# Kernel tuning notes

Hardware: AMD Instinct MI355X
Metric: run time of the kernel (lower is better)

## Reference

```python
import jax, jax.numpy as jnp
import numpy as np

D_MODEL = 1024
N_HEADS = 16
HEAD_DIM = D_MODEL // N_HEADS
NEG_INF = -1e30


def _rotary(v):
    # v: [B, H, T, hd]. Original module rotates each (even, odd) pair by 90 deg:
    # out[..., 2i] = -v[..., 2i+1]; out[..., 2i+1] = v[..., 2i]
    v2 = v.reshape(*v.shape[:-1], HEAD_DIM // 2, 2)
    return jnp.stack([-v2[..., 1], v2[..., 0]], axis=-1).reshape(v.shape)


def setup_inputs() -> dict:
    key = jax.random.key(0)
    ks = jax.random.split(key, 9)
    B, T, D = 2, 2048, D_MODEL
    s = 1.0 / np.sqrt(D)
    inp = {
        "x": jax.random.normal(ks[0], (B, T, D), dtype=jnp.float32),
        "Wq_w": jax.random.normal(ks[1], (D, D), dtype=jnp.float32) * s,
        "Wq_b": jnp.zeros((D,), dtype=jnp.float32),
        "Wk_w": jax.random.normal(ks[2], (D, D), dtype=jnp.float32) * s,
        "Wk_b": jnp.zeros((D,), dtype=jnp.float32),
        "Wv_w": jax.random.normal(ks[3], (D, D), dtype=jnp.float32) * s,
        "Wv_b": jnp.zeros((D,), dtype=jnp.float32),
        "Wo_w": jax.random.normal(ks[4], (D, D), dtype=jnp.float32) * s,
        "Wo_b": jnp.zeros((D,), dtype=jnp.float32),
    }
    # create_sparse_mask: block-diagonal True windows of size T//4
    window = T // 4
    blk = jnp.arange(T) // window
    inp["sparse_mask"] = blk[:, None] == blk[None, :]
    return inp


def reference(x, Wq_w, Wq_b, Wk_w, Wk_b, Wv_w, Wv_b, Wo_w, Wo_b, sparse_mask):
    B, T, D = x.shape
    H, hd = N_HEADS, HEAD_DIM

    def proj(w, b):  # [B,T,D] -> [B,H,T,hd]
        return (x @ w.T + b).reshape(B, T, H, hd).transpose(0, 2, 1, 3)

    q = _rotary(proj(Wq_w, Wq_b))
    k = _rotary(proj(Wk_w, Wk_b))
    v = proj(Wv_w, Wv_b)

    scores = jnp.einsum("bhqd,bhkd->bhqk", q, k) / jnp.sqrt(jnp.asarray(hd, x.dtype))
    causal = jnp.tril(jnp.ones((T, T), dtype=bool))
    allowed = sparse_mask & causal  # block-diagonal AND causal
    scores = jnp.where(allowed, scores, NEG_INF)
    attn = jax.nn.softmax(scores, axis=-1)  # dropout_p=0.1 omitted (eval mode)
    out = jnp.einsum("bhqk,bhkd->bhqd", attn, v)
    out = out.transpose(0, 2, 1, 3).reshape(B, T, D)
    return out @ Wo_w.T + Wo_b
```

## Files before the change

### kernel.cpp

```cpp
#include <hip/hip_runtime.h>
#include <hip/hip_bf16.h>
#include <stdint.h>

typedef __attribute__((ext_vector_type(4))) float f32x4;
typedef __attribute__((ext_vector_type(8))) __bf16 bf16x8;
typedef __attribute__((ext_vector_type(4))) unsigned short u16x4;
typedef __attribute__((ext_vector_type(8))) unsigned short u16x8;
typedef __attribute__((ext_vector_type(2))) unsigned int u32x2;
typedef const __attribute__((address_space(1))) void* as1_cvp;
typedef __attribute__((address_space(3))) void* as3_vp;

#define LOG2E 1.44269504088896340736f

#define VMW0() asm volatile("s_waitcnt vmcnt(0)" ::: "memory")
#define BAR()  do { __builtin_amdgcn_sched_barrier(0); __builtin_amdgcn_s_barrier(); \
                    __builtin_amdgcn_sched_barrier(0); } while (0)

static __device__ __forceinline__ unsigned short f2bf(float f) {
  union { float f; unsigned int u; } c; c.f = f;
  unsigned int r = c.u + 0x7FFFu + ((c.u >> 16) & 1u);
  return (unsigned short)(r >> 16);
}

static __device__ __forceinline__ void gl_lds16(const void* g, void* l) {
  __builtin_amdgcn_global_load_lds((as1_cvp)(uintptr_t)g, (as3_vp)(uintptr_t)l, 16, 0, 0);
}

__global__ __launch_bounds__(256) void cvt_kernel(
    const float* __restrict__ x, const float* __restrict__ wq, const float* __restrict__ wk,
    const float* __restrict__ wv, const float* __restrict__ wo,
    unsigned short* __restrict__ xb, unsigned short* __restrict__ wqb,
    unsigned short* __restrict__ wkb, unsigned short* __restrict__ wvb,
    unsigned short* __restrict__ wob) {
  long e = ((long)blockIdx.x * 256 + threadIdx.x) * 8;
  const float* s; unsigned short* d; long o;
  if (e < 4194304)      { s = x;  d = xb;  o = e; }
  else if (e < 5242880) { s = wq; d = wqb; o = e - 4194304; }
  else if (e < 6291456) { s = wk; d = wkb; o = e - 5242880; }
  else if (e < 7340032) { s = wv; d = wvb; o = e - 6291456; }
  else                  { s = wo; d = wob; o = e - 7340032; }
  float4 a = *(const float4*)(s + o);
  float4 b = *(const float4*)(s + o + 4);
  u16x8 v;
  v[0] = f2bf(a.x); v[1] = f2bf(a.y); v[2] = f2bf(a.z); v[3] = f2bf(a.w);
  v[4] = f2bf(b.x); v[5] = f2bf(b.y); v[6] = f2bf(b.z); v[7] = f2bf(b.w);
  *(u16x8*)(d + o) = v;
}

__global__ __launch_bounds__(512, 6) void gemm_qkv8(
    const unsigned short* __restrict__ xb, const unsigned short* __restrict__ wcat,
    const float* __restrict__ bq, const float* __restrict__ bk, const float* __restrict__ bv,
    unsigned short* __restrict__ qo, unsigned short* __restrict__ ko,
    unsigned short* __restrict__ vto) {
  __shared__ __align__(16) char lds[32768];
  const int tid = threadIdx.x;
  const int lane = tid & 63, wid = tid >> 6;
  const int wm = wid >> 2, wn = wid & 3;
  const int c = lane & 15, g = lane >> 4;

  const int bid = blockIdx.x;
  const int xcd = bid & 7, idx = bid >> 3;
  const int m0 = (((xcd & 1) << 4) + idx / 6) << 7;
  const int n0 = (((xcd >> 1) * 6) + idx % 6) << 7;

  const int sj = tid >> 3;
  const int sg = (tid & 7) ^ (sj & 7);
  const long soff = (((long)(sj + ((sg >> 2) << 6))) << 11) + ((sg & 3) << 4);
  const char* Ab = (const char*)xb;
  const char* Bb = (const char*)wcat;

  const int sA = ((((wm << 2) | g) ^ (c & 7)) << 4);
  const int sB = (((((wn >> 1) << 2) | g) ^ (c & 7)) << 4);
  const char* pAr = lds + (c << 7) + sA;
  const char* pBr = lds + 8192 + ((((wn & 1) << 5) + c) << 7) + sB;

  f32x4 acc[4][2] = {};

  auto STAGE = [&](int t, int slot) {
    char* db = lds + slot * 16384;
    const long ko = (long)t << 6;
    gl_lds16(Ab + ((long)m0 << 11) + soff + ko, db + tid * 16);
    gl_lds16(Bb + ((long)n0 << 11) + soff + ko, db + 8192 + tid * 16);
  };

  STAGE(0, 0);

#pragma unroll 1
  for (int t = 0; t < 32; ++t) {
    VMW0();
    BAR();
    if (t + 1 < 32) STAGE(t + 1, (t + 1) & 1);

    const int sb = (t & 1) * 16384;
    bf16x8 aa[4];
#pragma unroll
    for (int f = 0; f < 4; ++f) aa[f] = *(const bf16x8*)(pAr + sb + (f << 11));
    bf16x8 bb0 = *(const bf16x8*)(pBr + sb);
    bf16x8 bb1 = *(const bf16x8*)(pBr + sb + 2048);
    __builtin_amdgcn_s_setprio(1);
#pragma unroll
    for (int f = 0; f < 4; ++f)
      acc[f][0] = __builtin_amdgcn_mfma_f32_16x16x32_bf16(aa[f], bb0, acc[f][0], 0, 0, 0);
#pragma unroll
    for (int f = 0; f < 4; ++f)
      acc[f][1] = __builtin_amdgcn_mfma_f32_16x16x32_bf16(aa[f], bb1, acc[f][1], 0, 0, 0);
    __builtin_amdgcn_s_setprio(0);
  }

#pragma unroll
  for (int nf = 0; nf < 2; ++nf) {
    const int n = n0 + (wn << 5) + (nf << 4) + c;
    const int z = n >> 10, nn = n & 1023;
    const float bb_ = (z == 0 ? bq : z == 1 ? bk : bv)[nn];
    const float sc = (z == 0) ? 0.125f : 1.0f;
    const int h = nn >> 6, dd = nn & 63;
#pragma unroll
    for (int f = 0; f < 4; ++f) {
      const int mb = m0 + (wm << 6) + (f << 4) + (g << 2);
      const int b = mb >> 11, tt = mb & 2047;
      if (z < 2) {
        unsigned short* dst = (z == 0 ? qo : ko) +
            ((((long)(b << 4) + h) << 11) + tt) * 64 + dd;
#pragma unroll
        for (int j = 0; j < 4; ++j) dst[(long)j * 64] = f2bf((acc[f][nf][j] + bb_) * sc);
      } else {
        u16x4 pk;
#pragma unroll
        for (int j = 0; j < 4; ++j) pk[j] = f2bf(acc[f][nf][j] + bb_);
        *(u16x4*)(vto + ((((long)((b << 4) + h) << 6) + dd) << 11) + tt) = pk;
      }
    }
  }
}

__global__ __launch_bounds__(512, 4) void gemm_oproj8(
    const unsigned short* __restrict__ ab, const unsigned short* __restrict__ wob,
    const float* __restrict__ bo, float* __restrict__ out) {
  __shared__ __align__(16) char lds[49152];
  const int tid = threadIdx.x;
  const int lane = tid & 63, wid = tid >> 6;
  const int wm = wid >> 2, wn = wid & 3;
  const int c = lane & 15, g = lane >> 4;

  const int bid = blockIdx.x;
  const int xcd = bid & 7, idx = bid >> 3;
  const int m0 = ((xcd << 3) + (idx >> 3)) << 6;
  const int n0 = (idx & 7) << 7;

  const int srow = tid >> 3;
  const int coff = (((tid & 7) ^ (srow & 7)) << 4);
  const char* Ab = (const char*)ab;
  const char* Bb = (const char*)wob;

  const int swzr0 = ((g ^ (c & 7)) << 4);
  const int swzr1 = (((4 | g) ^ (c & 7)) << 4);

  f32x4 acc[2][2] = {};

  auto STAGE = [&](int kt, int unit) {
    char* db = lds + (kt & 1) * 24576;
    const char* gp; char* dst;
    if (unit == 0) {
      gp = Ab + ((long)(m0 + srow) << 11) + (kt << 7) + coff;
      dst = db + tid * 16;
    } else {
      gp = Bb + ((long)(n0 + (unit - 1) * 64 + srow) << 11) + (kt << 7) + coff;
      dst = db + unit * 8192 + tid * 16;
    }
    gl_lds16(gp, dst);
  };

  STAGE(0, 0); STAGE(0, 1); STAGE(0, 2);
  VMW0();
  BAR();

#pragma unroll 1
  for (int kt = 0; kt < 16; ++kt) {
    const int bufb = (kt & 1) * 24576;
    if (kt < 15) { STAGE(kt + 1, 0); STAGE(kt + 1, 1); STAGE(kt + 1, 2); }
    bf16x8 aa[2][2];
    const char* pA = lds + bufb + (wm << 12) + (c << 7);
#pragma unroll
    for (int f = 0; f < 2; ++f) {
      aa[f][0] = *(const bf16x8*)(pA + (f << 11) + swzr0);
      aa[f][1] = *(const bf16x8*)(pA + (f << 11) + swzr1);
    }
#pragma unroll
    for (int nf = 0; nf < 2; ++nf) {
      const int rB = (wn << 5) + (nf << 4) + c;
      const char* pB = lds + bufb + 8192 + ((rB >> 6) << 13) + ((rB & 63) << 7);
      bf16x8 b0 = *(const bf16x8*)(pB + swzr0);
      bf16x8 b1 = *(const bf16x8*)(pB + swzr1);
      __builtin_amdgcn_s_setprio(1);
#pragma unroll
      for (int f = 0; f < 2; ++f)
        acc[f][nf] = __builtin_amdgcn_mfma_f32_16x16x32_bf16(aa[f][0], b0, acc[f][nf], 0, 0, 0);
#pragma unroll
      for (int f = 0; f < 2; ++f)
        acc[f][nf] = __builtin_amdgcn_mfma_f32_16x16x32_bf16(aa[f][1], b1, acc[f][nf], 0, 0, 0);
      __builtin_amdgcn_s_setprio(0);
    }
    if (kt < 15) VMW0();
    BAR();
  }

#pragma unroll
  for (int nf = 0; nf < 2; ++nf) {
    const int n = n0 + (wn << 5) + (nf << 4) + c;
    const float bb = bo[n];
#pragma unroll
    for (int f = 0; f < 2; ++f) {
      const int mb = m0 + (wm << 5) + (f << 4) + (g << 2);
#pragma unroll
      for (int j = 0; j < 4; ++j)
        out[((long)(mb + j) << 10) + n] = acc[f][nf][j] + bb;
    }
  }
}

__global__ __launch_bounds__(512, 6) void attn_kernel(
    const unsigned short* __restrict__ qg, const unsigned short* __restrict__ kg,
    const unsigned short* __restrict__ vtg, unsigned short* __restrict__ og) {
  __shared__ __align__(16) char kv_s[2][16384];
  __shared__ __align__(16) char p_s[8][2304];

  const int bx = blockIdx.x, bh = blockIdx.y;
  const int map1[16] = {3,7,11,15, 2,6,10,14, 0,4,8,12, 1,5,9,13};
  const int map2[16] = {0,4,8,12, 1,5,9,13, 3,7,11,15, 2,6,10,14};
  const int qt = (bh < 16) ? map1[bx] : map2[bx];
  const int tid = threadIdx.x;
  const int lane = tid & 63, w = tid >> 6;
  const int c = lane & 15, g = lane >> 4;
  const int q0 = qt << 7;
  const int wstart = q0 & ~511;
  const int nt = ((q0 - wstart) >> 6) + 2;

  const unsigned short* qrow = qg + (((long)bh << 11) + q0 + (w << 4) + c) * 64;
  bf16x8 qa0 = *(const bf16x8*)(qrow + (g << 3));
  bf16x8 qa1 = *(const bf16x8*)(qrow + (g << 3) + 32);

  float m_run = -3.0e38f, l_run = 0.0f;
  f32x4 oacc[4] = {};

  const int sr = tid >> 3;
  const int jx16 = (((tid & 7) ^ (sr & 7)) << 4);
  const char* kbase = (const char*)kg + ((((long)bh << 11) + sr) << 7) + jx16;
  const char* vbase = (const char*)vtg + ((((long)bh << 6) + sr) << 12) + jx16;
  const int t16 = tid << 4;

  auto STAGEKV = [&](int kv0, int bsel) {
    char* dst = kv_s[bsel];
    gl_lds16(kbase + ((long)kv0 << 7), dst + t16);
    gl_lds16(vbase + ((long)kv0 << 1), dst + 8192 + t16);
  };

  STAGEKV(wstart, 0);

  for (int t = 0; t < nt; ++t) {
    VMW0();
    BAR();
    if (t + 1 < nt) STAGEKV(wstart + ((t + 1) << 6), (t + 1) & 1);

    const char* kb_ = kv_s[t & 1];
    const char* vb_ = kv_s[t & 1] + 8192;
    const int kv0 = wstart + (t << 6);

    f32x4 sacc[4] = {};
    __builtin_amdgcn_s_setprio(1);
#pragma unroll
    for (int mf = 0; mf < 4; ++mf) {
      const int kr = (mf << 4) + c;
      const char* kp = kb_ + (kr << 7);
      bf16x8 k0 = *(const bf16x8*)(kp + ((g ^ (kr & 7)) << 4));
      bf16x8 k1 = *(const bf16x8*)(kp + (((4 | g) ^ (kr & 7)) << 4));
      sacc[mf] = __builtin_amdgcn_mfma_f32_16x16x32_bf16(k0, qa0, sacc[mf], 0, 0, 0);
      sacc[mf] = __builtin_amdgcn_mfma_f32_16x16x32_bf16(k1, qa1, sacc[mf], 0, 0, 0);
    }
    __builtin_amdgcn_s_setprio(0);

    const int dkv = kv0 - q0;
    if (dkv > (w << 4) - 64) {
      const int qrel = (w << 4) + c;
#pragma unroll
      for (int mf = 0; mf < 4; ++mf)
#pragma unroll
        for (int j = 0; j < 4; ++j)
          if (dkv + (mf << 4) + (g << 2) + j > qrel) sacc[mf][j] = -3.0e38f;
    }

    float pm[4];
#pragma unroll
    for (int mf = 0; mf < 4; ++mf)
      pm[mf] = fmaxf(fmaxf(sacc[mf][0], sacc[mf][1]), fmaxf(sacc[mf][2], sacc[mf][3]));
    float pmax = fmaxf(fmaxf(pm[0], pm[1]), fmaxf(pm[2], pm[3]));
    pmax = fmaxf(pmax, __shfl_xor(pmax, 16));
    pmax = fmaxf(pmax, __shfl_xor(pmax, 32));

    const bool resc = !__all(pmax <= m_run + 8.0f);
    const float m_new = resc ? fmaxf(m_run, pmax) : m_run;

    const float mL = m_new * LOG2E;
    float ls[4];
#pragma unroll
    for (int mf = 0; mf < 4; ++mf) {
      float p0 = __builtin_amdgcn_exp2f(__builtin_fmaf(sacc[mf][0], LOG2E, -mL));
      float p1 = __builtin_amdgcn_exp2f(__builtin_fmaf(sacc[mf][1], LOG2E, -mL));
      float p2 = __builtin_amdgcn_exp2f(__builtin_fmaf(sacc[mf][2], LOG2E, -mL));
      float p3 = __builtin_amdgcn_exp2f(__builtin_fmaf(sacc[mf][3], LOG2E, -mL));
      sacc[mf][0] = p0; sacc[mf][1] = p1; sacc[mf][2] = p2; sacc[mf][3] = p3;
      ls[mf] = (p0 + p1) + (p2 + p3);
    }
    float lsum = (ls[0] + ls[1]) + (ls[2] + ls[3]);
    lsum += __shfl_xor(lsum, 16);
    lsum += __shfl_xor(lsum, 32);

    if (resc) {
      const float alpha = __builtin_amdgcn_exp2f((m_run - m_new) * LOG2E);
      l_run *= alpha;
#pragma unroll
      for (int j = 0; j < 4; ++j) {
        const float aj = __shfl(alpha, (g << 2) + j);
#pragma unroll
        for (int nf = 0; nf < 4; ++nf) oacc[nf][j] *= aj;
      }
      m_run = m_new;
    }
    l_run += lsum;

    {
      char* pw = p_s[w] + c * 144;
#pragma unroll
      for (int mf = 0; mf < 4; ++mf) {
        unsigned int p01, p23;
        asm("v_cvt_pk_bf16_f32 %0, %1, %2" : "=v"(p01) : "v"(sacc[mf][0]), "v"(sacc[mf][1]));
        asm("v_cvt_pk_bf16_f32 %0, %1, %2" : "=v"(p23) : "v"(sacc[mf][2]), "v"(sacc[mf][3]));
        u32x2 pk; pk[0] = p01; pk[1] = p23;
        *(u32x2*)(pw + (mf << 5) + (g << 3)) = pk;
      }
    }

    const char* pr = p_s[w] + c * 144;
    __builtin_amdgcn_s_setprio(1);
#pragma unroll
    for (int kk = 0; kk < 2; ++kk) {
      bf16x8 pa = *(const bf16x8*)(pr + (kk << 6) + (g << 4));
#pragma unroll
      for (int nf = 0; nf < 4; ++nf) {
        const int vr = (nf << 4) + c;
        bf16x8 vb = *(const bf16x8*)(vb_ + (vr << 7) +
                                     ((((kk << 2) | g) ^ (vr & 7)) << 4));
        oacc[nf] = __builtin_amdgcn_mfma_f32_16x16x32_bf16(pa, vb, oacc[nf], 0, 0, 0);
      }
    }
    __builtin_amdgcn_s_setprio(0);
  }

  const int b = bh >> 4, h = bh & 15;
#pragma unroll
  for (int j = 0; j < 4; ++j) {
    const float linv = 1.0f / __shfl(l_run, (g << 2) + j);
    const int trow = q0 + (w << 4) + (g << 2) + j;
    unsigned short* dst = og + ((((long)(b << 11)) + trow) << 10) + (h << 6);
#pragma unroll
    for (int nf = 0; nf < 4; ++nf)
      dst[(nf << 4) + c] = f2bf(oacc[nf][j] * linv);
  }
}

extern "C" void kernel_launch(void* const* d_in, const int* in_sizes, int n_in,
                              void* d_out, int out_size, void* d_ws, size_t ws_size,
                              hipStream_t stream) {
  const float* x  = (const float*)d_in[0];
  const float* wq = (const float*)d_in[1];
  const float* bq = (const float*)d_in[2];
  const float* wk = (const float*)d_in[3];
  const float* bk = (const float*)d_in[4];
  const float* wv = (const float*)d_in[5];
  const float* bv = (const float*)d_in[6];
  const float* wo = (const float*)d_in[7];
  const float* bo = (const float*)d_in[8];

  char* ws = (char*)d_ws;
  unsigned short* xb    = (unsigned short*)(ws);
  unsigned short* wqb   = (unsigned short*)(ws + 8388608);
  unsigned short* wkb   = (unsigned short*)(ws + 10485760);
  unsigned short* wvb   = (unsigned short*)(ws + 12582912);
  unsigned short* wob   = (unsigned short*)(ws + 14680064);
  unsigned short* qb    = (unsigned short*)(ws + 16777216);
  unsigned short* kb    = (unsigned short*)(ws + 25165824);
  unsigned short* vtb   = (unsigned short*)(ws + 33554432);
  unsigned short* attnb = xb;

  cvt_kernel<<<4096, 256, 0, stream>>>(x, wq, wk, wv, wo, xb, wqb, wkb, wvb, wob);
  gemm_qkv8<<<768, 512, 0, stream>>>(xb, wqb, bq, bk, bv, qb, kb, vtb);
  attn_kernel<<<dim3(16, 32), 512, 0, stream>>>(qb, kb, vtb, attnb);
  gemm_oproj8<<<512, 512, 0, stream>>>(attnb, wob, bo, (float*)d_out);
}
```

Baseline: 79.59 us.

## Enlarge QKV GEMM tiles to 256x256 with deeper quarter-staged LDS pipeline

Measured after the change: 78.63 us. Within noise of the previous version (-1.2%).

```diff
diff --git a/kernel.cpp b/kernel.cpp
--- a/kernel.cpp
+++ b/kernel.cpp
@@ -13,8 +13,12 @@
 #define LOG2E 1.44269504088896340736f
 
 #define VMW0() asm volatile("s_waitcnt vmcnt(0)" ::: "memory")
+#define VMW6() asm volatile("s_waitcnt vmcnt(6)" ::: "memory")
 #define BAR()  do { __builtin_amdgcn_sched_barrier(0); __builtin_amdgcn_s_barrier(); \
                     __builtin_amdgcn_sched_barrier(0); } while (0)
+#define SB()   __builtin_amdgcn_s_barrier()
+#define LGKM0() do { asm volatile("s_waitcnt lgkmcnt(0)" ::: "memory"); \
+                     __builtin_amdgcn_sched_barrier(0); } while (0)
 
 static __device__ __forceinline__ unsigned short f2bf(float f) {
   union { float f; unsigned int u; } c; c.f = f;
@@ -47,86 +51,129 @@
   *(u16x8*)(d + o) = v;
 }
 
-__global__ __launch_bounds__(512, 6) void gemm_qkv8(
+__global__ __launch_bounds__(512, 2) void gemm_qkv8(
     const unsigned short* __restrict__ xb, const unsigned short* __restrict__ wcat,
     const float* __restrict__ bq, const float* __restrict__ bk, const float* __restrict__ bv,
     unsigned short* __restrict__ qo, unsigned short* __restrict__ ko,
     unsigned short* __restrict__ vto) {
-  __shared__ __align__(16) char lds[32768];
+  __shared__ __align__(16) char lds[131072];
   const int tid = threadIdx.x;
   const int lane = tid & 63, wid = tid >> 6;
   const int wm = wid >> 2, wn = wid & 3;
   const int c = lane & 15, g = lane >> 4;
 
   const int bid = blockIdx.x;
-  const int xcd = bid & 7, idx = bid >> 3;
-  const int m0 = (((xcd & 1) << 4) + idx / 6) << 7;
-  const int n0 = (((xcd >> 1) * 6) + idx % 6) << 7;
-
-  const int sj = tid >> 3;
-  const int sg = (tid & 7) ^ (sj & 7);
-  const long soff = (((long)(sj + ((sg >> 2) << 6))) << 11) + ((sg & 3) << 4);
+  const int swz = (bid & 7) * 24 + (bid >> 3);
+  const int n0 = (swz % 12) << 8;
+  const int m0 = (swz / 12) << 8;
+
+  const int srow = tid >> 3;
+  const int coff = (((tid & 7) ^ (srow & 7)) << 4);
   const char* Ab = (const char*)xb;
   const char* Bb = (const char*)wcat;
 
-  const int sA = ((((wm << 2) | g) ^ (c & 7)) << 4);
-  const int sB = (((((wn >> 1) << 2) | g) ^ (c & 7)) << 4);
-  const char* pAr = lds + (c << 7) + sA;
-  const char* pBr = lds + 8192 + ((((wn & 1) << 5) + c) << 7) + sB;
-
-  f32x4 acc[4][2] = {};
-
-  auto STAGE = [&](int t, int slot) {
-    char* db = lds + slot * 16384;
-    const long ko = (long)t << 6;
-    gl_lds16(Ab + ((long)m0 << 11) + soff + ko, db + tid * 16);
-    gl_lds16(Bb + ((long)n0 << 11) + soff + ko, db + 8192 + tid * 16);
-  };
-
-  STAGE(0, 0);
+  const int swzr0 = ((g ^ (c & 7)) << 4);
+  const int swzr1 = (((4 | g) ^ (c & 7)) << 4);
+  const int aRow = ((wm << 6) + c) << 7;
+  const int bRow = 32768 + (((wn << 5) + c) << 7);
+
+  f32x4 acc[8][4] = {};
+  bf16x8 aa[4][2], bb[2][2][2];
+
+  auto STAGE = [&](int H) {
+    const int part = H & 3, kt = H >> 2;
+    char* db = lds + ((kt & 1) << 16);
+    const char* mat; int rb, reg;
+    if (part == 0)      { mat = Ab; rb = m0;       reg = 0; }
+    else if (part == 1) { mat = Bb; rb = n0;       reg = 32768; }
+    else if (part == 2) { mat = Bb; rb = n0 + 128; reg = 49152; }
+    else                { mat = Ab; rb = m0 + 128; reg = 16384; }
+    const char* gp = mat + ((long)(rb + srow) << 11) + (kt << 7) + coff;
+    gl_lds16(gp,               db + reg + tid * 16);
+    gl_lds16(gp + (64l << 11), db + reg + 8192 + tid * 16);
+  };
+  auto RDA = [&](int bufb, int half) {
+    const char* p = lds + bufb + (half << 14) + aRow;
+#pragma unroll
+    for (int m4 = 0; m4 < 4; ++m4) {
+      aa[m4][0] = *(const bf16x8*)(p + (m4 << 11) + swzr0);
+      aa[m4][1] = *(const bf16x8*)(p + (m4 << 11) + swzr1);
+    }
+  };
+  auto RDB = [&](int bufb, int half) {
+    const char* p = lds + bufb + (half << 14) + bRow;
+#pragma unroll
+    for (int n2 = 0; n2 < 2; ++n2) {
+      bb[half][n2][0] = *(const bf16x8*)(p + (n2 << 11) + swzr0);
+      bb[half][n2][1] = *(const bf16x8*)(p + (n2 << 11) + swzr1);
+    }
+  };
+  auto MM = [&](int mh, int nh) {
+    __builtin_amdgcn_s_setprio(1);
+#pragma unroll
+    for (int m4 = 0; m4 < 4; ++m4)
+#pragma unroll
+      for (int n2 = 0; n2 < 2; ++n2)
+#pragma unroll
+        for (int kf = 0; kf < 2; ++kf)
+          acc[mh * 4 + m4][nh * 2 + n2] = __builtin_amdgcn_mfma_f32_16x16x32_bf16(
+              aa[m4][kf], bb[nh][n2][kf], acc[mh * 4 + m4][nh * 2 + n2], 0, 0, 0);
+    __builtin_amdgcn_s_setprio(0);
+  };
+
+  STAGE(0); STAGE(1); STAGE(2); STAGE(3); STAGE(4);
+  VMW6();
+  SB();
 
 #pragma unroll 1
-  for (int t = 0; t < 32; ++t) {
-    VMW0();
-    BAR();
-    if (t + 1 < 32) STAGE(t + 1, (t + 1) & 1);
-
-    const int sb = (t & 1) * 16384;
-    bf16x8 aa[4];
-#pragma unroll
-    for (int f = 0; f < 4; ++f) aa[f] = *(const bf16x8*)(pAr + sb + (f << 11));
-    bf16x8 bb0 = *(const bf16x8*)(pBr + sb);
-    bf16x8 bb1 = *(const bf16x8*)(pBr + sb + 2048);
-    __builtin_amdgcn_s_setprio(1);
-#pragma unroll
-    for (int f = 0; f < 4; ++f)
-      acc[f][0] = __builtin_amdgcn_mfma_f32_16x16x32_bf16(aa[f], bb0, acc[f][0], 0, 0, 0);
-#pragma unroll
-    for (int f = 0; f < 4; ++f)
-      acc[f][1] = __builtin_amdgcn_mfma_f32_16x16x32_bf16(aa[f], bb1, acc[f][1], 0, 0, 0);
-    __builtin_amdgcn_s_setprio(0);
-  }
-
-#pragma unroll
-  for (int nf = 0; nf < 2; ++nf) {
-    const int n = n0 + (wn << 5) + (nf << 4) + c;
+  for (int kt = 0; kt < 16; ++kt) {
+    const int bufb = (kt & 1) << 16;
+    const int GP = kt << 2;
+    RDA(bufb, 0); RDB(bufb, 0);
+    STAGE(GP + 5);
+    VMW6();
+    SB(); LGKM0();
+    MM(0, 0);
+    SB();
+    RDB(bufb, 1);
+    STAGE(GP + 6);
+    VMW6();
+    SB(); LGKM0();
+    MM(0, 1);
+    SB();
+    RDA(bufb, 1);
+    STAGE(GP + 7);
+    SB(); LGKM0();
+    MM(1, 1);
+    SB();
+    STAGE(GP + 8);
+    VMW6();
+    SB(); LGKM0();
+    MM(1, 0);
+    SB();
+  }
+  VMW0();
+
+#pragma unroll
+  for (int nf = 0; nf < 4; ++nf) {
+    const int n = n0 + ((nf >> 1) << 7) + (wn << 5) + ((nf & 1) << 4) + c;
     const int z = n >> 10, nn = n & 1023;
     const float bb_ = (z == 0 ? bq : z == 1 ? bk : bv)[nn];
     const float sc = (z == 0) ? 0.125f : 1.0f;
     const int h = nn >> 6, dd = nn & 63;
 #pragma unroll
-    for (int f = 0; f < 4; ++f) {
-      const int mb = m0 + (wm << 6) + (f << 4) + (g << 2);
+    for (int mf = 0; mf < 8; ++mf) {
+      const int mb = m0 + ((mf >> 2) << 7) + (wm << 6) + ((mf & 3) << 4) + (g << 2);
       const int b = mb >> 11, tt = mb & 2047;
       if (z < 2) {
         unsigned short* dst = (z == 0 ? qo : ko) +
             ((((long)(b << 4) + h) << 11) + tt) * 64 + dd;
 #pragma unroll
-        for (int j = 0; j < 4; ++j) dst[(long)j * 64] = f2bf((acc[f][nf][j] + bb_) * sc);
+        for (int j = 0; j < 4; ++j) dst[(long)j * 64] = f2bf((acc[mf][nf][j] + bb_) * sc);
       } else {
         u16x4 pk;
 #pragma unroll
-        for (int j = 0; j < 4; ++j) pk[j] = f2bf(acc[f][nf][j] + bb_);
+        for (int j = 0; j < 4; ++j) pk[j] = f2bf(acc[mf][nf][j] + bb_);
         *(u16x4*)(vto + ((((long)((b << 4) + h) << 6) + dd) << 11) + tt) = pk;
       }
     }
@@ -392,7 +439,7 @@
   unsigned short* attnb = xb;
 
   cvt_kernel<<<4096, 256, 0, stream>>>(x, wq, wk, wv, wo, xb, wqb, wkb, wvb, wob);
-  gemm_qkv8<<<768, 512, 0, stream>>>(xb, wqb, bq, bk, bv, qb, kb, vtb);
+  gemm_qkv8<<<192, 512, 0, stream>>>(xb, wqb, bq, bk, bv, qb, kb, vtb);
   attn_kernel<<<dim3(16, 32), 512, 0, stream>>>(qb, kb, vtb, attnb);
   gemm_oproj8<<<512, 512, 0, stream>>>(attnb, wob, bo, (float*)d_out);
 }
```

## Rework QKV GEMM to 256-thread blocks with 64x64 warp tiles, single-buffered

Applied to the files above, without the earlier changes.

New measurement: 80.29 us. Within noise of the previous version (+0.9%).

```diff
diff --git a/kernel.cpp b/kernel.cpp
--- a/kernel.cpp
+++ b/kernel.cpp
@@ -47,86 +47,80 @@
   *(u16x8*)(d + o) = v;
 }
 
-__global__ __launch_bounds__(512, 6) void gemm_qkv8(
+__global__ __launch_bounds__(256, 3) void gemm_qkv97(
     const unsigned short* __restrict__ xb, const unsigned short* __restrict__ wcat,
     const float* __restrict__ bq, const float* __restrict__ bk, const float* __restrict__ bv,
     unsigned short* __restrict__ qo, unsigned short* __restrict__ ko,
     unsigned short* __restrict__ vto) {
-  __shared__ __align__(16) char lds[32768];
+  __shared__ __align__(16) char lds[16384];
   const int tid = threadIdx.x;
   const int lane = tid & 63, wid = tid >> 6;
-  const int wm = wid >> 2, wn = wid & 3;
+  const int wm = wid >> 1, wn = wid & 1;
   const int c = lane & 15, g = lane >> 4;
 
   const int bid = blockIdx.x;
   const int xcd = bid & 7, idx = bid >> 3;
-  const int m0 = (((xcd & 1) << 4) + idx / 6) << 7;
-  const int n0 = (((xcd >> 1) * 6) + idx % 6) << 7;
+  const int m0 = (((xcd >> 1) << 3) + idx / 12) << 7;
+  const int n0 = (((xcd & 1) * 12) + idx % 12) << 7;
 
   const int sj = tid >> 3;
   const int sg = (tid & 7) ^ (sj & 7);
-  const long soff = (((long)(sj + ((sg >> 2) << 6))) << 11) + ((sg & 3) << 4);
-  const char* Ab = (const char*)xb;
-  const char* Bb = (const char*)wcat;
+  const long rowoff = ((long)(sj + ((sg >> 2) << 6)) << 11) + ((sg & 3) << 4);
+  const char* Ag = (const char*)xb   + ((long)m0 << 11) + rowoff;
+  const char* Bg = (const char*)wcat + ((long)n0 << 11) + rowoff;
 
   const int sA = ((((wm << 2) | g) ^ (c & 7)) << 4);
-  const int sB = (((((wn >> 1) << 2) | g) ^ (c & 7)) << 4);
+  const int sB = ((((wn << 2) | g) ^ (c & 7)) << 4);
   const char* pAr = lds + (c << 7) + sA;
-  const char* pBr = lds + 8192 + ((((wn & 1) << 5) + c) << 7) + sB;
-
-  f32x4 acc[4][2] = {};
-
-  auto STAGE = [&](int t, int slot) {
-    char* db = lds + slot * 16384;
-    const long ko = (long)t << 6;
-    gl_lds16(Ab + ((long)m0 << 11) + soff + ko, db + tid * 16);
-    gl_lds16(Bb + ((long)n0 << 11) + soff + ko, db + 8192 + tid * 16);
-  };
-
-  STAGE(0, 0);
+  const char* pBr = lds + 8192 + (c << 7) + sB;
+
+  f32x4 acc[4][4] = {};
 
 #pragma unroll 1
-  for (int t = 0; t < 32; ++t) {
+  for (int kt = 0; kt < 32; ++kt) {
+    const long ko = (long)kt << 6;
+    gl_lds16(Ag + ko,               lds + tid * 16);
+    gl_lds16(Ag + ko + (32l << 11), lds + 4096 + tid * 16);
+    gl_lds16(Bg + ko,               lds + 8192 + tid * 16);
+    gl_lds16(Bg + ko + (32l << 11), lds + 12288 + tid * 16);
     VMW0();
     BAR();
-    if (t + 1 < 32) STAGE(t + 1, (t + 1) & 1);
-
-    const int sb = (t & 1) * 16384;
-    bf16x8 aa[4];
-#pragma unroll
-    for (int f = 0; f < 4; ++f) aa[f] = *(const bf16x8*)(pAr + sb + (f << 11));
-    bf16x8 bb0 = *(const bf16x8*)(pBr + sb);
-    bf16x8 bb1 = *(const bf16x8*)(pBr + sb + 2048);
+
+    bf16x8 aa[4], bb[4];
+#pragma unroll
+    for (int mf = 0; mf < 4; ++mf) aa[mf] = *(const bf16x8*)(pAr + (mf << 11));
+#pragma unroll
+    for (int nf = 0; nf < 4; ++nf) bb[nf] = *(const bf16x8*)(pBr + (nf << 11));
     __builtin_amdgcn_s_setprio(1);
 #pragma unroll
-    for (int f = 0; f < 4; ++f)
-      acc[f][0] = __builtin_amdgcn_mfma_f32_16x16x32_bf16(aa[f], bb0, acc[f][0], 0, 0, 0);
-#pragma unroll
-    for (int f = 0; f < 4; ++f)
-      acc[f][1] = __builtin_amdgcn_mfma_f32_16x16x32_bf16(aa[f], bb1, acc[f][1], 0, 0, 0);
+    for (int mf = 0; mf < 4; ++mf)
+#pragma unroll
+      for (int nf = 0; nf < 4; ++nf)
+        acc[mf][nf] = __builtin_amdgcn_mfma_f32_16x16x32_bf16(aa[mf], bb[nf], acc[mf][nf], 0, 0, 0);
     __builtin_amdgcn_s_setprio(0);
-  }
-
-#pragma unroll
-  for (int nf = 0; nf < 2; ++nf) {
-    const int n = n0 + (wn << 5) + (nf << 4) + c;
+    BAR();
+  }
+
+#pragma unroll
+  for (int nf = 0; nf < 4; ++nf) {
+    const int n = n0 + (wn << 6) + (nf << 4) + c;
     const int z = n >> 10, nn = n & 1023;
     const float bb_ = (z == 0 ? bq : z == 1 ? bk : bv)[nn];
     const float sc = (z == 0) ? 0.125f : 1.0f;
     const int h = nn >> 6, dd = nn & 63;
 #pragma unroll
-    for (int f = 0; f < 4; ++f) {
-      const int mb = m0 + (wm << 6) + (f << 4) + (g << 2);
+    for (int mf = 0; mf < 4; ++mf) {
+      const int mb = m0 + (wm << 6) + (mf << 4) + (g << 2);
       const int b = mb >> 11, tt = mb & 2047;
       if (z < 2) {
         unsigned short* dst = (z == 0 ? qo : ko) +
             ((((long)(b << 4) + h) << 11) + tt) * 64 + dd;
 #pragma unroll
-        for (int j = 0; j < 4; ++j) dst[(long)j * 64] = f2bf((acc[f][nf][j] + bb_) * sc);
+        for (int j = 0; j < 4; ++j) dst[(long)j * 64] = f2bf((acc[mf][nf][j] + bb_) * sc);
       } else {
         u16x4 pk;
 #pragma unroll
-        for (int j = 0; j < 4; ++j) pk[j] = f2bf(acc[f][nf][j] + bb_);
+        for (int j = 0; j < 4; ++j) pk[j] = f2bf(acc[mf][nf][j] + bb_);
         *(u16x4*)(vto + ((((long)((b << 4) + h) << 6) + dd) << 11) + tt) = pk;
       }
     }
@@ -392,7 +386,7 @@
   unsigned short* attnb = xb;
 
   cvt_kernel<<<4096, 256, 0, stream>>>(x, wq, wk, wv, wo, xb, wqb, wkb, wvb, wob);
-  gemm_qkv8<<<768, 512, 0, stream>>>(xb, wqb, bq, bk, bv, qb, kb, vtb);
+  gemm_qkv97<<<768, 256, 0, stream>>>(xb, wqb, bq, bk, bv, qb, kb, vtb);
   attn_kernel<<<dim3(16, 32), 512, 0, stream>>>(qb, kb, vtb, attnb);
   gemm_oproj8<<<512, 512, 0, stream>>>(attnb, wob, bo, (float*)d_out);
 }
```
